# Performance work log

Measured on AMD Instinct MI355X. Metric: run time of the kernel, lower is better.

The kernel has to match this reference:

```python
import jax, jax.numpy as jnp
import numpy as np
import math

EPS = 1e-5

def _ln(x, w, b):
    m = jnp.mean(x, axis=-1, keepdims=True)
    v = jnp.mean((x - m) ** 2, axis=-1, keepdims=True)
    return (x - m) * jax.lax.rsqrt(v + EPS) * w + b

def setup_inputs() -> dict:
    key = jax.random.key(0)
    L, E, V, T, B = 8, 1024, 32000, 1024, 4
    ks = jax.random.split(key, 9)
    f = lambda k, s: jax.random.normal(k, s, dtype=jnp.float32) * 0.02
    return dict(
        idx=jax.random.randint(ks[0], (B, T), 0, V),
        wte=f(ks[1], (V, E)),
        wpe=f(ks[2], (T, E)),
        ln1_w=jnp.ones((L, E), jnp.float32), ln1_b=jnp.zeros((L, E), jnp.float32),
        attn_w=f(ks[3], (L, 3 * E, E)), attn_b=jnp.zeros((L, 3 * E), jnp.float32),
        proj_w=f(ks[4], (L, E, E)), proj_b=jnp.zeros((L, E), jnp.float32),
        ln2_w=jnp.ones((L, E), jnp.float32), ln2_b=jnp.zeros((L, E), jnp.float32),
        fc_w=f(ks[5], (L, 4 * E, E)), fc_b=jnp.zeros((L, 4 * E), jnp.float32),
        fc2_w=f(ks[6], (L, E, 4 * E)), fc2_b=jnp.zeros((L, E), jnp.float32),
        lnf_w=jnp.ones((E,), jnp.float32), lnf_b=jnp.zeros((E,), jnp.float32),
        lm_head_w=f(ks[7], (V, E)),
        n_head=16,
    )

def reference(idx, wte, wpe, ln1_w, ln1_b, attn_w, attn_b, proj_w, proj_b,
              ln2_w, ln2_b, fc_w, fc_b, fc2_w, fc2_b, lnf_w, lnf_b,
              lm_head_w, n_head):
    B, T = idx.shape
    E = wte.shape[1]
    H = int(n_head)
    hd = E // H
    scale = 1.0 / math.sqrt(hd)
    x = wte[idx] + wpe[:T]  # [B,T,E]
    causal = jnp.tril(jnp.ones((T, T), dtype=bool))
    neg_inf = jnp.float32(-jnp.inf)

    def body(x, p):
        l1w, l1b, Wa, ba, Wp, bp, l2w, l2b, Wf, bf, W2, b2 = p
        h = _ln(x, l1w, l1b)
        qkv = h @ Wa.T + ba  # [B,T,3E]
        q, k, v = jnp.split(qkv, 3, axis=-1)
        q = q.reshape(B, T, H, hd)
        k = k.reshape(B, T, H, hd)
        v = v.reshape(B, T, H, hd)
        att = jnp.einsum('bqhd,bkhd->bhqk', q, k) * scale
        att = jnp.where(causal, att, neg_inf)
        att = jax.nn.softmax(att, axis=-1)  # dropout is identity in eval
        y = jnp.einsum('bhqk,bkhd->bqhd', att, v).reshape(B, T, E)
        x = x + (y @ Wp.T + bp)
        h2 = _ln(x, l2w, l2b)
        mlp = jax.nn.gelu(h2 @ Wf.T + bf, approximate=False) @ W2.T + b2
        return x + mlp, None

    params = (ln1_w, ln1_b, attn_w, attn_b, proj_w, proj_b,
              ln2_w, ln2_b, fc_w, fc_b, fc2_w, fc2_b)
    x, _ = jax.lax.scan(body, x, params)
    x = _ln(x, lnf_w, lnf_b)
    logits = x @ lm_head_w.T  # [B,T,V]
    return logits
```

## Files before the change

### kernel.cpp

```cpp
#include <hip/hip_runtime.h>

typedef __bf16 bf16x8 __attribute__((ext_vector_type(8)));
typedef float  f32x4  __attribute__((ext_vector_type(4)));
typedef short  s16x8  __attribute__((ext_vector_type(8)));
typedef unsigned int u32;
#define AS1 __attribute__((address_space(1)))
#define AS3 __attribute__((address_space(3)))

#define E_ 1024
#define T_ 1024
#define B_ 4
#define L_ 8
#define V_ 32000
#define M_ (B_*T_)

static __device__ __forceinline__ ushort f2bf(float f) {
  return __builtin_bit_cast(ushort, (__bf16)f);
}

__global__ __launch_bounds__(256) void castall_k(
    const float* __restrict__ a0, const float* __restrict__ a1,
    const float* __restrict__ a2, const float* __restrict__ a3,
    const float* __restrict__ a4,
    ushort* __restrict__ o0, ushort* __restrict__ o1, ushort* __restrict__ o2,
    ushort* __restrict__ o3, ushort* __restrict__ o4) {
  int bid = blockIdx.x;
  const float* in; ushort* out; int base;
  if (bid < 12288)      { in = a0; out = o0; base = bid; }
  else if (bid < 16384) { in = a1; out = o1; base = bid - 12288; }
  else if (bid < 32768) { in = a2; out = o2; base = bid - 16384; }
  else if (bid < 49152) { in = a3; out = o3; base = bid - 32768; }
  else                  { in = a4; out = o4; base = bid - 49152; }
  size_t i = ((size_t)base * 256 + threadIdx.x) * 8;
  float4 a = *(const float4*)(in + i);
  float4 b = *(const float4*)(in + i + 4);
  float v[8] = {a.x, a.y, a.z, a.w, b.x, b.y, b.z, b.w};
  union { s16x8 v; ushort u[8]; } pk;
  #pragma unroll
  for (int j = 0; j < 8; ++j) pk.u[j] = f2bf(v[j]);
  *(s16x8*)(out + i) = pk.v;
}

static __device__ __forceinline__ void ln_core(float4 v, int t,
    const float* __restrict__ w, const float* __restrict__ b,
    ushort* __restrict__ out, size_t row) {
  float s  = v.x + v.y + v.z + v.w;
  float s2 = v.x*v.x + v.y*v.y + v.z*v.z + v.w*v.w;
  #pragma unroll
  for (int o = 32; o > 0; o >>= 1) { s += __shfl_down(s, o); s2 += __shfl_down(s2, o); }
  __shared__ float sh[8];
  int wv = t >> 6;
  if ((t & 63) == 0) { sh[wv] = s; sh[4 + wv] = s2; }
  __syncthreads();
  s  = sh[0] + sh[1] + sh[2] + sh[3];
  s2 = sh[4] + sh[5] + sh[6] + sh[7];
  float mean = s * (1.f / E_);
  float var  = s2 * (1.f / E_) - mean * mean;
  float inv  = rsqrtf(var + 1e-5f);
  float4 wv4 = ((const float4*)w)[t];
  float4 bv4 = ((const float4*)b)[t];
  ushort* op = out + row * E_ + t * 4;
  op[0] = f2bf((v.x - mean) * inv * wv4.x + bv4.x);
  op[1] = f2bf((v.y - mean) * inv * wv4.y + bv4.y);
  op[2] = f2bf((v.z - mean) * inv * wv4.z + bv4.z);
  op[3] = f2bf((v.w - mean) * inv * wv4.w + bv4.w);
}

__global__ __launch_bounds__(256) void embedln_k(const int* __restrict__ idx,
    const float* __restrict__ wte, const float* __restrict__ wpe,
    const float* __restrict__ w, const float* __restrict__ b,
    float* __restrict__ x, ushort* __restrict__ out) {
  int row = blockIdx.x;
  int tok = idx[row];
  int t = row & (T_ - 1);
  int c = threadIdx.x;
  float4 a = ((const float4*)(wte + (size_t)tok * E_))[c];
  float4 p = ((const float4*)(wpe + (size_t)t * E_))[c];
  float4 v; v.x = a.x + p.x; v.y = a.y + p.y; v.z = a.z + p.z; v.w = a.w + p.w;
  ((float4*)(x + (size_t)row * E_))[c] = v;
  ln_core(v, c, w, b, out, (size_t)row);
}

__global__ __launch_bounds__(256) void ln_k(const float* __restrict__ x,
    const float* __restrict__ w, const float* __restrict__ b,
    ushort* __restrict__ out) {
  int row = blockIdx.x;
  int t = threadIdx.x;
  float4 v = ((const float4*)(x + (size_t)row * E_))[t];
  ln_core(v, t, w, b, out, (size_t)row);
}

__global__ __launch_bounds__(256) void redln_k(const float* __restrict__ p,
    const float* __restrict__ bias, float* __restrict__ x,
    const float* __restrict__ w, const float* __restrict__ b,
    ushort* __restrict__ out) {
  int row = blockIdx.x;
  int t = threadIdx.x;
  float4 v = ((const float4*)(x + (size_t)row * E_))[t];
  float4 bb = ((const float4*)bias)[t];
  v.x += bb.x; v.y += bb.y; v.z += bb.z; v.w += bb.w;
  #pragma unroll
  for (int sk = 0; sk < 4; ++sk) {
    float4 q = ((const float4*)(p + ((size_t)sk * M_ + row) * E_))[t];
    v.x += q.x; v.y += q.y; v.z += q.z; v.w += q.w;
  }
  ((float4*)(x + (size_t)row * E_))[t] = v;
  ln_core(v, t, w, b, out, (size_t)row);
}

#define BAR() do { __builtin_amdgcn_s_barrier(); __builtin_amdgcn_sched_barrier(0); } while (0)

template<int BUF, int SLOT, int RBV, int VM, typename F>
static __device__ __forceinline__ void phase2(
    const ushort (&AL)[32768], const ushort (&BL)[32768],
    bf16x8 (&av)[4][2], bf16x8 (&bv)[4][2],
    int arow, int brow, int ca0, int ca1, f32x4 (&acc)[8][4], F&& stage) {
  #pragma unroll
  for (int mfi = 0; mfi < 4; ++mfi) {
    av[mfi][0] = __builtin_bit_cast(bf16x8, *(const s16x8*)&AL[(BUF*2+SLOT)*8192 + arow + mfi*1024 + ca0]);
    av[mfi][1] = __builtin_bit_cast(bf16x8, *(const s16x8*)&AL[(BUF*2+SLOT)*8192 + arow + mfi*1024 + ca1]);
  }
  if (RBV) {
    #pragma unroll
    for (int nfi = 0; nfi < 2; ++nfi) {
      bv[nfi][0]     = __builtin_bit_cast(bf16x8, *(const s16x8*)&BL[(BUF*2+0)*8192 + brow + nfi*1024 + ca0]);
      bv[nfi][1]     = __builtin_bit_cast(bf16x8, *(const s16x8*)&BL[(BUF*2+0)*8192 + brow + nfi*1024 + ca1]);
      bv[2 + nfi][0] = __builtin_bit_cast(bf16x8, *(const s16x8*)&BL[(BUF*2+1)*8192 + brow + nfi*1024 + ca0]);
      bv[2 + nfi][1] = __builtin_bit_cast(bf16x8, *(const s16x8*)&BL[(BUF*2+1)*8192 + brow + nfi*1024 + ca1]);
    }
  }
  stage();
  BAR();
  __builtin_amdgcn_s_setprio(1);
  #pragma unroll
  for (int ks = 0; ks < 2; ++ks)
    #pragma unroll
    for (int mfi = 0; mfi < 4; ++mfi)
      #pragma unroll
      for (int nfi = 0; nfi < 4; ++nfi)
        acc[SLOT*4+mfi][nfi] = __builtin_amdgcn_mfma_f32_16x16x32_bf16(
            av[mfi][ks], bv[nfi][ks], acc[SLOT*4+mfi][nfi], 0, 0, 0);
  __builtin_amdgcn_s_setprio(0);
  if (VM) asm volatile("s_waitcnt vmcnt(4)");
  BAR();
}

#define GLDS(src, dst) __builtin_amdgcn_global_load_lds((const AS1 u32*)(src), (AS3 u32*)(dst), 16, 0, 0)
#define STAGE_A(b, s, t) do { \
  GLDS(ap##s##_0 + (size_t)(t)*64, &AL[((b)*2+(s))*8192 + w*512]); \
  GLDS(ap##s##_1 + (size_t)(t)*64, &AL[((b)*2+(s))*8192 + 4096 + w*512]); } while(0)
#define STAGE_B(b, s, t) do { \
  GLDS(bp##s##_0 + (size_t)(t)*64, &BL[((b)*2+(s))*8192 + w*512]); \
  GLDS(bp##s##_1 + (size_t)(t)*64, &BL[((b)*2+(s))*8192 + 4096 + w*512]); } while(0)

template<int EPI>
static __device__ __forceinline__
void gemm8_body(const ushort* __restrict__ A, const ushort* __restrict__ W,
                const float* __restrict__ bias,
                float* __restrict__ outf, ushort* __restrict__ outh,
                ushort* __restrict__ qb, ushort* __restrict__ kb, ushort* __restrict__ vb,
                int M, int N, int K, int Kst) {
  __shared__ __align__(16) ushort AL[32768];
  __shared__ __align__(16) ushort BL[32768];
  int id  = blockIdx.x;
  int sk = 0, bx, by;
  if (EPI == 4) {
    sk = id >> 6; int rem = id & 63; bx = rem & 3; by = rem >> 2;
  } else {
    int nwg = gridDim.x;
    int swz = (id & 7) * (nwg >> 3) + (id >> 3);
    bx = swz >> 4; by = swz & 15;
  }
  int bm = by * 256, bn = bx * 256;
  int tid = threadIdx.x;
  int w = tid >> 6, lane = tid & 63;
  int wm = w >> 2, wn = w & 3;
  int g = lane >> 4, lr = lane & 15;
  int sl8 = lane >> 3, sc = lane & 7;
  int cg8 = (sc ^ sl8) * 8;

  const ushort* Ab = A + (size_t)sk * K;
  const ushort* Wb = W + (size_t)sk * K;
  int r0 = w * 8 + sl8;
  const ushort* ap0_0 = Ab + (size_t)(bm +       0 + r0) * Kst + cg8;
  const ushort* ap0_1 = Ab + (size_t)(bm + 128 + 0 + r0) * Kst + cg8;
  const ushort* ap1_0 = Ab + (size_t)(bm +      64 + r0) * Kst + cg8;
  const ushort* ap1_1 = Ab + (size_t)(bm + 128 + 64 + r0) * Kst + cg8;
  int sr0 = r0, sr1 = 64 + r0;
  const ushort* bp0_0 = Wb + (size_t)(bn + (sr0 >> 5) * 64 +  0 + (sr0 & 31)) * Kst + cg8;
  const ushort* bp0_1 = Wb + (size_t)(bn + (sr1 >> 5) * 64 +  0 + (sr1 & 31)) * Kst + cg8;
  const ushort* bp1_0 = Wb + (size_t)(bn + (sr0 >> 5) * 64 + 32 + (sr0 & 31)) * Kst + cg8;
  const ushort* bp1_1 = Wb + (size_t)(bn + (sr1 >> 5) * 64 + 32 + (sr1 & 31)) * Kst + cg8;

  int NT = K >> 6;
  int NITER = NT >> 1;
  int arow = (wm * 64 + lr) * 64;
  int brow = (wn * 32 + lr) * 64;
  int ca0 = ((0 + g) ^ (lr & 7)) * 8;
  int ca1 = ((4 + g) ^ (lr & 7)) * 8;
  f32x4 acc[8][4] = {};
  bf16x8 av[4][2], bv[4][2];

  STAGE_A(0, 0, 0); STAGE_A(0, 1, 0); STAGE_B(0, 0, 0); STAGE_B(0, 1, 0);
  STAGE_A(1, 0, 1); STAGE_B(1, 0, 1);
  asm volatile("s_waitcnt vmcnt(0)" ::: "memory");
  BAR();

  for (int i = 0; i < NITER; ++i) {
    int t1 = 2 * i + 1;
    int t2 = 2 * i + 2; if (t2 > NT - 1) t2 = NT - 1;
    int t3 = 2 * i + 3; if (t3 > NT - 1) t3 = NT - 1;
    phase2<0,0,1,0>(AL, BL, av, bv, arow, brow, ca0, ca1, acc,
                    [&]{ STAGE_A(1, 1, t1); STAGE_B(1, 1, t1); });
    phase2<0,1,0,1>(AL, BL, av, bv, arow, brow, ca0, ca1, acc,
                    [&]{ STAGE_A(0, 0, t2); STAGE_B(0, 0, t2); });
    phase2<1,0,1,0>(AL, BL, av, bv, arow, brow, ca0, ca1, acc,
                    [&]{ STAGE_A(0, 1, t2); STAGE_B(0, 1, t2); });
    phase2<1,1,0,1>(AL, BL, av, bv, arow, brow, ca0, ca1, acc,
                    [&]{ STAGE_A(1, 0, t3); STAGE_B(1, 0, t3); });
  }

  if (EPI == 3 && (bn >> 10) == 2) {
    #pragma unroll
    for (int mf = 0; mf < 8; ++mf) {
      int row = bm + wm * 128 + mf * 16 + g * 4;
      int b = row >> 10, t = row & 1023;
      #pragma unroll
      for (int nf = 0; nf < 4; ++nf) {
        int col = bn + wn * 64 + nf * 16 + lr;
        int cc = col & 1023;
        int h = cc >> 6, d = cc & 63;
        float bs = bias[col];
        union { ushort u[4]; uint2 v; } pk4;
        #pragma unroll
        for (int reg = 0; reg < 4; ++reg) pk4.u[reg] = f2bf(acc[mf][nf][reg] + bs);
        *(uint2*)&vb[((size_t)(b * 16 + h) * 64 + d) * T_ + t] = pk4.v;
      }
    }
    return;
  }

  ushort* dst = nullptr; float scl = 1.f;
  if (EPI == 3) {
    int sec = bn >> 10;
    dst = (sec == 0) ? qb : kb;
    scl = (sec == 0) ? 0.125f : 1.f;
  }
  #pragma unroll
  for (int mf = 0; mf < 8; ++mf) {
    #pragma unroll
    for (int reg = 0; reg < 4; ++reg) {
      int row = bm + wm * 128 + mf * 16 + g * 4 + reg;
      #pragma unroll
      for (int nf = 0; nf < 4; ++nf) {
        int col = bn + wn * 64 + nf * 16 + lr;
        float v = acc[mf][nf][reg];
        if (bias) v += bias[col];
        if (EPI == 0) {
          outf[(size_t)row * N + col] = v;
        } else if (EPI == 2) {
          float gl = 0.5f * v * (1.f + erff(v * 0.70710678118654752f));
          outh[(size_t)row * N + col] = f2bf(gl);
        } else if (EPI == 4) {
          outf[((size_t)sk * M + row) * N + col] = v;
        } else {
          int b = row >> 10, t = row & 1023;
          int cc = col & 1023;
          int h = cc >> 6, d = cc & 63;
          dst[((size_t)(b * 16 + h) * T_ + t) * 64 + d] = f2bf(v * scl);
        }
      }
    }
  }
}

__global__ __launch_bounds__(512, 2)
void gemm8_qkv(const ushort* A, const ushort* W, const float* bias,
               ushort* qb, ushort* kb, ushort* vtb) {
  gemm8_body<3>(A, W, bias, nullptr, nullptr, qb, kb, vtb, M_, 3 * E_, E_, E_);
}
__global__ __launch_bounds__(512, 2)
void gemm8_fc(const ushort* A, const ushort* W, const float* bias, ushort* outh) {
  gemm8_body<2>(A, W, bias, nullptr, outh, nullptr, nullptr, nullptr, M_, 4 * E_, E_, E_);
}
__global__ __launch_bounds__(512, 2)
void gemm8_lm(const ushort* A, const ushort* W, float* outf) {
  gemm8_body<0>(A, W, nullptr, outf, nullptr, nullptr, nullptr, nullptr, M_, V_, E_, E_);
}
__global__ __launch_bounds__(512, 2)
void gemm8_sk(const ushort* A, const ushort* W, float* pbuf) {
  gemm8_body<4>(A, W, nullptr, pbuf, nullptr, nullptr, nullptr, nullptr, M_, E_, E_, 4 * E_);
}

__global__ __launch_bounds__(256, 4)
void gbt2_proj(const ushort* __restrict__ A, const ushort* __restrict__ W,
               const float* __restrict__ bias, const float* __restrict__ res,
               float* __restrict__ outf) {
  __shared__ __align__(16) ushort As[128 * 64];
  __shared__ __align__(16) ushort Ws[128 * 64];
  const int N = E_, K = E_;
  int id  = blockIdx.x;
  int nwg = gridDim.x;
  int swz = (id & 7) * (nwg >> 3) + (id >> 3);
  int bx = swz >> 5, by = swz & 31;
  int bm = by * 128, bn = bx * 128;
  int tid  = threadIdx.x;
  int wave = tid >> 6, lane = tid & 63;
  int wr = wave >> 1, wc = wave & 1;
  int g  = lane >> 4, lr = lane & 15;
  int sl8 = lane >> 3, sc = lane & 7;
  int cg8 = (sc ^ sl8) * 8;
  int r0 = wave * 8 + sl8;

  const ushort* ap = A + (size_t)(bm + r0) * K + cg8;
  const ushort* wp = W + (size_t)(bn + r0) * K + cg8;
  f32x4 acc[4][4] = {};

  for (int k0 = 0; k0 < K; k0 += 64) {
    #pragma unroll
    for (int j = 0; j < 4; ++j) {
      GLDS(ap + (size_t)(j * 32) * K + k0, &As[(wave * 8 + j * 32) * 64]);
      GLDS(wp + (size_t)(j * 32) * K + k0, &Ws[(wave * 8 + j * 32) * 64]);
    }
    __syncthreads();
    #pragma unroll
    for (int ks = 0; ks < 2; ++ks) {
      int ca = ((ks * 4 + g) ^ (lr & 7)) * 8;
      bf16x8 af[4], bfr[4];
      #pragma unroll
      for (int f = 0; f < 4; ++f) {
        af[f]  = __builtin_bit_cast(bf16x8, *(const s16x8*)&As[(wr * 64 + f * 16 + lr) * 64 + ca]);
        bfr[f] = __builtin_bit_cast(bf16x8, *(const s16x8*)&Ws[(wc * 64 + f * 16 + lr) * 64 + ca]);
      }
      #pragma unroll
      for (int mf = 0; mf < 4; ++mf)
        #pragma unroll
        for (int nf = 0; nf < 4; ++nf)
          acc[mf][nf] = __builtin_amdgcn_mfma_f32_16x16x32_bf16(af[mf], bfr[nf], acc[mf][nf], 0, 0, 0);
    }
    __syncthreads();
  }

  #pragma unroll
  for (int mf = 0; mf < 4; ++mf)
    #pragma unroll
    for (int reg = 0; reg < 4; ++reg) {
      int row = bm + wr * 64 + mf * 16 + g * 4 + reg;
      #pragma unroll
      for (int nf = 0; nf < 4; ++nf) {
        int col = bn + wc * 64 + nf * 16 + lr;
        float v = acc[mf][nf][reg] + bias[col];
        outf[(size_t)row * N + col] = v + res[(size_t)row * N + col];
      }
    }
}

static __device__ __forceinline__ void sm_step(
    f32x4 (&s)[4], float& m, float& l, f32x4 (&acc)[4], bf16x8 (&ap)[2],
    int qrow, int kbase0, bool diag, int g) {
  if (diag) {
    #pragma unroll
    for (int nf = 0; nf < 4; ++nf)
      #pragma unroll
      for (int reg = 0; reg < 4; ++reg)
        if (kbase0 + nf * 16 + g * 4 + reg > qrow) s[nf][reg] = -INFINITY;
  }
  float pmax = s[0][0];
  #pragma unroll
  for (int nf = 0; nf < 4; ++nf)
    #pragma unroll
    for (int reg = 0; reg < 4; ++reg) pmax = fmaxf(pmax, s[nf][reg]);
  pmax = fmaxf(pmax, __shfl_xor(pmax, 16));
  pmax = fmaxf(pmax, __shfl_xor(pmax, 32));
  if (__any(pmax > m + 8.f)) {
    float mn = fmaxf(m, pmax);
    float corr = __expf(m - mn);
    m = mn; l *= corr;
    #pragma unroll
    for (int reg = 0; reg < 4; ++reg) {
      float cc = __shfl(corr, g * 4 + reg);
      #pragma unroll
      for (int nfd = 0; nfd < 4; ++nfd) acc[nfd][reg] *= cc;
    }
  }
  float ps = 0.f;
  union { bf16x8 v[2]; ushort u[16]; } pk;
  #pragma unroll
  for (int nf = 0; nf < 4; ++nf)
    #pragma unroll
    for (int reg = 0; reg < 4; ++reg) {
      float pv = __expf(s[nf][reg] - m);
      ps += pv;
      pk.u[nf * 4 + reg] = f2bf(pv);
    }
  ps += __shfl_xor(ps, 16);
  ps += __shfl_xor(ps, 32);
  l += ps;
  ap[0] = pk.v[0];
  ap[1] = pk.v[1];
}

#define LOADK(dst, kt) do { \
  _Pragma("unroll") \
  for (int ks_ = 0; ks_ < 2; ++ks_) \
    _Pragma("unroll") \
    for (int nf_ = 0; nf_ < 4; ++nf_) \
      dst[ks_][nf_] = __builtin_bit_cast(bf16x8, *(const s16x8*)( \
          kbase + (size_t)((kt) * 64 + nf_ * 16 + lr) * 64 + ks_ * 32 + g * 8)); \
} while (0)

#define LOADV(dst, kt) do { \
  _Pragma("unroll") \
  for (int ks_ = 0; ks_ < 2; ++ks_) \
    _Pragma("unroll") \
    for (int nf_ = 0; nf_ < 4; ++nf_) { \
      const ushort* vp_ = vbase + (size_t)(nf_ * 16 + lr) * T_ + (kt) * 64 + ks_ * 32 + g * 4; \
      uint2 vlo_ = *(const uint2*)vp_; \
      uint2 vhi_ = *(const uint2*)(vp_ + 16); \
      union { uint4 u; bf16x8 v; } bb_; \
      bb_.u = make_uint4(vlo_.x, vlo_.y, vhi_.x, vhi_.y); \
      dst[ks_][nf_] = bb_.v; \
    } \
} while (0)

#define TILE(KF) do { \
  bool diag_ = (kt == nkt - 1); \
  f32x4 s0[4] = {}, s1[4] = {}; \
  _Pragma("unroll") \
  for (int ks_ = 0; ks_ < 2; ++ks_) \
    _Pragma("unroll") \
    for (int nf_ = 0; nf_ < 4; ++nf_) { \
      s0[nf_] = __builtin_amdgcn_mfma_f32_16x16x32_bf16(KF[ks_][nf_], aq[0][ks_], s0[nf_], 0, 0, 0); \
      s1[nf_] = __builtin_amdgcn_mfma_f32_16x16x32_bf16(KF[ks_][nf_], aq[1][ks_], s1[nf_], 0, 0, 0); \
    } \
  bf16x8 ap0[2], ap1[2]; \
  sm_step(s0, m0, l0, accO[0], ap0, qbase + 0 * 16 + lr, kt * 64, diag_, g); \
  sm_step(s1, m1, l1, accO[1], ap1, qbase + 1 * 16 + lr, kt * 64, diag_, g); \
  _Pragma("unroll") \
  for (int ks_ = 0; ks_ < 2; ++ks_) \
    _Pragma("unroll") \
    for (int nf_ = 0; nf_ < 4; ++nf_) { \
      accO[0][nf_] = __builtin_amdgcn_mfma_f32_16x16x32_bf16(ap0[ks_], vf[ks_][nf_], accO[0][nf_], 0, 0, 0); \
      accO[1][nf_] = __builtin_amdgcn_mfma_f32_16x16x32_bf16(ap1[ks_], vf[ks_][nf_], accO[1][nf_], 0, 0, 0); \
    } \
} while (0)

__global__ __launch_bounds__(64) void attn_k(const ushort* __restrict__ Qg,
    const ushort* __restrict__ Kg, const ushort* __restrict__ Vg,
    ushort* __restrict__ y) {
  int bh = blockIdx.x;
  int qt = blockIdx.y;
  int lane = threadIdx.x;
  int g = lane >> 4, lr = lane & 15;
  int qbase = qt * 32;

  const ushort* kbase = Kg + (size_t)bh * T_ * 64;
  const ushort* vbase = Vg + (size_t)bh * 64 * T_;

  bf16x8 aq[2][2];
  #pragma unroll
  for (int st = 0; st < 2; ++st) {
    const ushort* qp = Qg + ((size_t)bh * T_ + qbase + st * 16 + lr) * 64;
    aq[st][0] = __builtin_bit_cast(bf16x8, *(const s16x8*)(qp + g * 8));
    aq[st][1] = __builtin_bit_cast(bf16x8, *(const s16x8*)(qp + 32 + g * 8));
  }

  f32x4 accO[2][4] = {};
  float m0 = -INFINITY, m1 = -INFINITY, l0 = 0.f, l1 = 0.f;

  int nkt = (qbase >> 6) + 1;
  bf16x8 kA[2][4], kB[2][4], vf[2][4];
  LOADK(kA, 0);
  int kt = 0;
  for (;;) {
    LOADV(vf, kt);
    if (kt + 1 < nkt) LOADK(kB, kt + 1);
    TILE(kA);
    if (++kt >= nkt) break;
    LOADV(vf, kt);
    if (kt + 1 < nkt) LOADK(kA, kt + 1);
    TILE(kB);
    if (++kt >= nkt) break;
  }

  int b = bh >> 4, h = bh & 15;
  float li0 = 1.f / l0, li1 = 1.f / l1;
  #pragma unroll
  for (int st = 0; st < 2; ++st) {
    float lsrc = (st == 0) ? li0 : li1;
    #pragma unroll
    for (int reg = 0; reg < 4; ++reg) {
      float inv = __shfl(lsrc, g * 4 + reg);
      size_t row = (size_t)b * T_ + qbase + st * 16 + g * 4 + reg;
      #pragma unroll
      for (int nfd = 0; nfd < 4; ++nfd)
        y[row * E_ + h * 64 + nfd * 16 + lr] = f2bf(accO[st][nfd][reg] * inv);
    }
  }
}

extern "C" void kernel_launch(void* const* d_in, const int* in_sizes, int n_in,
                              void* d_out, int out_size, void* d_ws, size_t ws_size,
                              hipStream_t stream) {
  const int*   idx   = (const int*)  d_in[0];
  const float* wte   = (const float*)d_in[1];
  const float* wpe   = (const float*)d_in[2];
  const float* ln1w  = (const float*)d_in[3];
  const float* ln1b  = (const float*)d_in[4];
  const float* attnw = (const float*)d_in[5];
  const float* attnb = (const float*)d_in[6];
  const float* projw = (const float*)d_in[7];
  const float* projb = (const float*)d_in[8];
  const float* ln2w  = (const float*)d_in[9];
  const float* ln2b  = (const float*)d_in[10];
  const float* fcw   = (const float*)d_in[11];
  const float* fcb   = (const float*)d_in[12];
  const float* fc2w  = (const float*)d_in[13];
  const float* fc2b  = (const float*)d_in[14];
  const float* lnfw  = (const float*)d_in[15];
  const float* lnfb  = (const float*)d_in[16];
  const float* lmw   = (const float*)d_in[17];
  float* out = (float*)d_out;

  char* p = (char*)d_ws;
  auto take = [&](size_t bytes) { char* r = p; p += (bytes + 255) & ~(size_t)255; return r; };
  ushort* wb_attn = (ushort*)take((size_t)L_ * 3 * E_ * E_ * 2);
  ushort* wb_proj = (ushort*)take((size_t)L_ * E_ * E_ * 2);
  ushort* wb_fc   = (ushort*)take((size_t)L_ * 4 * E_ * E_ * 2);
  ushort* wb_fc2  = (ushort*)take((size_t)L_ * E_ * 4 * E_ * 2);
  ushort* wb_lm   = (ushort*)take((size_t)V_ * E_ * 2);
  float*  x       = (float*) take((size_t)M_ * E_ * 4);
  ushort* hbuf    = (ushort*)take((size_t)M_ * E_ * 2);
  ushort* qb      = (ushort*)take((size_t)B_ * 16 * T_ * 64 * 2);
  ushort* kbuf    = (ushort*)take((size_t)B_ * 16 * T_ * 64 * 2);
  ushort* vtb     = (ushort*)take((size_t)B_ * 16 * T_ * 64 * 2);
  ushort* ybuf    = (ushort*)take((size_t)M_ * E_ * 2);
  ushort* mlp     = (ushort*)take((size_t)M_ * 4 * E_ * 2);
  float*  pbuf    = (float*) take((size_t)4 * M_ * E_ * 4);

  castall_k<<<65152, 256, 0, stream>>>(attnw, projw, fcw, fc2w, lmw,
                                       wb_attn, wb_proj, wb_fc, wb_fc2, wb_lm);
  embedln_k<<<M_, 256, 0, stream>>>(idx, wte, wpe, ln1w, ln1b, x, hbuf);

  for (int l = 0; l < L_; ++l) {
    gemm8_qkv<<<(3 * E_ / 256) * (M_ / 256), 512, 0, stream>>>(
        hbuf, wb_attn + (size_t)l * 3 * E_ * E_, attnb + l * 3 * E_, qb, kbuf, vtb);
    attn_k<<<dim3(B_ * 16, 32), 64, 0, stream>>>(qb, kbuf, vtb, ybuf);
    gbt2_proj<<<(E_ / 128) * (M_ / 128), 256, 0, stream>>>(
        ybuf, wb_proj + (size_t)l * E_ * E_, projb + l * E_, x, x);
    ln_k<<<M_, 256, 0, stream>>>(x, ln2w + l * E_, ln2b + l * E_, hbuf);
    gemm8_fc<<<(4 * E_ / 256) * (M_ / 256), 512, 0, stream>>>(
        hbuf, wb_fc + (size_t)l * 4 * E_ * E_, fcb + l * 4 * E_, mlp);
    gemm8_sk<<<256, 512, 0, stream>>>(mlp, wb_fc2 + (size_t)l * E_ * 4 * E_, pbuf);
    if (l < L_ - 1)
      redln_k<<<M_, 256, 0, stream>>>(pbuf, fc2b + l * E_, x,
                                      ln1w + (l + 1) * E_, ln1b + (l + 1) * E_, hbuf);
    else
      redln_k<<<M_, 256, 0, stream>>>(pbuf, fc2b + l * E_, x, lnfw, lnfb, hbuf);
  }
  gemm8_lm<<<(V_ / 256) * (M_ / 256), 512, 0, stream>>>(hbuf, wb_lm, out);
}
```

Measured before the change: 2.665 ms.

## Split GEMM main loop into eight finer phases with quadrant-level MFMA scheduling

Restructures the GEMM main loop from four phases to eight. Each phase now computes one M-half by N-half quadrant of MFMAs and issues either the A or the B global-to-LDS stage load, not both. LDS reads now use inline-asm ds_read_b128 with an explicit lgkmcnt wait after the barrier. The goal is to interleave LDS reads, global loads and MFMA work more finely so memory latency is hidden, at the cost of twice as many barriers per iteration and more register state for the A and B fragments.

```diff
diff --git a/kernel.cpp b/kernel.cpp
--- a/kernel.cpp
+++ b/kernel.cpp
@@ -16,6 +16,13 @@
 
 static __device__ __forceinline__ ushort f2bf(float f) {
   return __builtin_bit_cast(ushort, (__bf16)f);
+}
+
+static __device__ __forceinline__ bf16x8 dsr(const ushort* p) {
+  u32 a = (u32)(size_t)(const AS3 ushort*)p;
+  bf16x8 d;
+  asm volatile("ds_read_b128 %0, %1" : "=v"(d) : "v"(a));
+  return d;
 }
 
 __global__ __launch_bounds__(256) void castall_k(
@@ -108,41 +115,42 @@
   ln_core(v, t, w, b, out, (size_t)row);
 }
 
-#define BAR() do { __builtin_amdgcn_s_barrier(); __builtin_amdgcn_sched_barrier(0); } while (0)
-
-template<int BUF, int SLOT, int RBV, int VM, typename F>
-static __device__ __forceinline__ void phase2(
-    const ushort (&AL)[32768], const ushort (&BL)[32768],
-    bf16x8 (&av)[4][2], bf16x8 (&bv)[4][2],
+template<int BUF, int MH, int NH, int RA, int RB, int VM, typename F>
+static __device__ __forceinline__ void ph8(
+    const ushort* AL, const ushort* BL,
+    bf16x8 (&av)[2][4][2], bf16x8 (&bv)[2][2][2],
     int arow, int brow, int ca0, int ca1, f32x4 (&acc)[8][4], F&& stage) {
-  #pragma unroll
-  for (int mfi = 0; mfi < 4; ++mfi) {
-    av[mfi][0] = __builtin_bit_cast(bf16x8, *(const s16x8*)&AL[(BUF*2+SLOT)*8192 + arow + mfi*1024 + ca0]);
-    av[mfi][1] = __builtin_bit_cast(bf16x8, *(const s16x8*)&AL[(BUF*2+SLOT)*8192 + arow + mfi*1024 + ca1]);
-  }
-  if (RBV) {
+  if (RA) {
+    #pragma unroll
+    for (int mfi = 0; mfi < 4; ++mfi) {
+      av[MH][mfi][0] = dsr(&AL[(BUF*2+MH)*8192 + arow + mfi*1024 + ca0]);
+      av[MH][mfi][1] = dsr(&AL[(BUF*2+MH)*8192 + arow + mfi*1024 + ca1]);
+    }
+  }
+  if (RB) {
     #pragma unroll
     for (int nfi = 0; nfi < 2; ++nfi) {
-      bv[nfi][0]     = __builtin_bit_cast(bf16x8, *(const s16x8*)&BL[(BUF*2+0)*8192 + brow + nfi*1024 + ca0]);
-      bv[nfi][1]     = __builtin_bit_cast(bf16x8, *(const s16x8*)&BL[(BUF*2+0)*8192 + brow + nfi*1024 + ca1]);
-      bv[2 + nfi][0] = __builtin_bit_cast(bf16x8, *(const s16x8*)&BL[(BUF*2+1)*8192 + brow + nfi*1024 + ca0]);
-      bv[2 + nfi][1] = __builtin_bit_cast(bf16x8, *(const s16x8*)&BL[(BUF*2+1)*8192 + brow + nfi*1024 + ca1]);
+      bv[NH][nfi][0] = dsr(&BL[(BUF*2+NH)*8192 + brow + nfi*1024 + ca0]);
+      bv[NH][nfi][1] = dsr(&BL[(BUF*2+NH)*8192 + brow + nfi*1024 + ca1]);
     }
   }
   stage();
-  BAR();
+  __builtin_amdgcn_s_barrier();
+  asm volatile("s_waitcnt lgkmcnt(0)");
+  __builtin_amdgcn_sched_barrier(0);
   __builtin_amdgcn_s_setprio(1);
   #pragma unroll
   for (int ks = 0; ks < 2; ++ks)
     #pragma unroll
     for (int mfi = 0; mfi < 4; ++mfi)
       #pragma unroll
-      for (int nfi = 0; nfi < 4; ++nfi)
-        acc[SLOT*4+mfi][nfi] = __builtin_amdgcn_mfma_f32_16x16x32_bf16(
-            av[mfi][ks], bv[nfi][ks], acc[SLOT*4+mfi][nfi], 0, 0, 0);
+      for (int nfi = 0; nfi < 2; ++nfi)
+        acc[MH*4+mfi][NH*2+nfi] = __builtin_amdgcn_mfma_f32_16x16x32_bf16(
+            av[MH][mfi][ks], bv[NH][nfi][ks], acc[MH*4+mfi][NH*2+nfi], 0, 0, 0);
   __builtin_amdgcn_s_setprio(0);
   if (VM) asm volatile("s_waitcnt vmcnt(4)");
-  BAR();
+  __builtin_amdgcn_s_barrier();
+  __builtin_amdgcn_sched_barrier(0);
 }
 
 #define GLDS(src, dst) __builtin_amdgcn_global_load_lds((const AS1 u32*)(src), (AS3 u32*)(dst), 16, 0, 0)
@@ -199,25 +207,26 @@
   int ca0 = ((0 + g) ^ (lr & 7)) * 8;
   int ca1 = ((4 + g) ^ (lr & 7)) * 8;
   f32x4 acc[8][4] = {};
-  bf16x8 av[4][2], bv[4][2];
+  bf16x8 av[2][4][2], bv[2][2][2];
 
   STAGE_A(0, 0, 0); STAGE_A(0, 1, 0); STAGE_B(0, 0, 0); STAGE_B(0, 1, 0);
   STAGE_A(1, 0, 1); STAGE_B(1, 0, 1);
   asm volatile("s_waitcnt vmcnt(0)" ::: "memory");
-  BAR();
+  __builtin_amdgcn_s_barrier();
+  __builtin_amdgcn_sched_barrier(0);
 
   for (int i = 0; i < NITER; ++i) {
     int t1 = 2 * i + 1;
     int t2 = 2 * i + 2; if (t2 > NT - 1) t2 = NT - 1;
     int t3 = 2 * i + 3; if (t3 > NT - 1) t3 = NT - 1;
-    phase2<0,0,1,0>(AL, BL, av, bv, arow, brow, ca0, ca1, acc,
-                    [&]{ STAGE_A(1, 1, t1); STAGE_B(1, 1, t1); });
-    phase2<0,1,0,1>(AL, BL, av, bv, arow, brow, ca0, ca1, acc,
-                    [&]{ STAGE_A(0, 0, t2); STAGE_B(0, 0, t2); });
-    phase2<1,0,1,0>(AL, BL, av, bv, arow, brow, ca0, ca1, acc,
-                    [&]{ STAGE_A(0, 1, t2); STAGE_B(0, 1, t2); });
-    phase2<1,1,0,1>(AL, BL, av, bv, arow, brow, ca0, ca1, acc,
-                    [&]{ STAGE_A(1, 0, t3); STAGE_B(1, 0, t3); });
+    ph8<0,0,0,1,1,0>(AL, BL, av, bv, arow, brow, ca0, ca1, acc, [&]{ STAGE_A(1, 1, t1); });
+    ph8<0,0,1,0,1,0>(AL, BL, av, bv, arow, brow, ca0, ca1, acc, [&]{ STAGE_B(1, 1, t1); });
+    ph8<0,1,1,1,0,0>(AL, BL, av, bv, arow, brow, ca0, ca1, acc, [&]{ STAGE_A(0, 0, t2); });
+    ph8<0,1,0,0,0,1>(AL, BL, av, bv, arow, brow, ca0, ca1, acc, [&]{ STAGE_B(0, 0, t2); });
+    ph8<1,0,0,1,1,0>(AL, BL, av, bv, arow, brow, ca0, ca1, acc, [&]{ STAGE_A(0, 1, t2); });
+    ph8<1,0,1,0,1,0>(AL, BL, av, bv, arow, brow, ca0, ca1, acc, [&]{ STAGE_B(0, 1, t2); });
+    ph8<1,1,1,1,0,0>(AL, BL, av, bv, arow, brow, ca0, ca1, acc, [&]{ STAGE_A(1, 0, t3); });
+    ph8<1,1,0,0,0,1>(AL, BL, av, bv, arow, brow, ca0, ca1, acc, [&]{ STAGE_B(1, 0, t3); });
   }
 
   if (EPI == 3 && (bn >> 10) == 2) {
```

New measurement: 2.516 ms. -5.6%, faster.
